# Kernel tuning notes

Measured on AMD Instinct MI355X. Metric: run time of the kernel, lower is better.

Reference implementation:

```python
import jax, jax.numpy as jnp
import numpy as np

N = 100000   # nodes
F_IN = 128   # node features
H = 32       # hidden size (hard-coded in module)


def setup_inputs() -> dict:
    key = jax.random.key(0)
    ks = jax.random.split(key, 20)
    inp = {
        'x': jax.random.normal(ks[0], (N, F_IN), dtype=jnp.float32),
        'edge_index': jax.random.randint(ks[1], (2, 3200000), 0, N, dtype=jnp.int64),
        'edge_weight': jax.random.uniform(ks[2], (3200000,), dtype=jnp.float32),
        'prev_hidden_state': jax.random.normal(ks[3], (N, H), dtype=jnp.float32),
    }
    s = 1.0 / np.sqrt(F_IN)
    s2 = 1.0 / np.sqrt(2 * H)
    sh = 1.0 / np.sqrt(H)
    # GCNConv weights (in->H) + bias, for gates z, r, h
    for i, g in enumerate(['z', 'r', 'h']):
        inp[f'Wc_{g}'] = jax.random.uniform(ks[4 + i], (F_IN, H), minval=-s, maxval=s, dtype=jnp.float32)
        inp[f'bc_{g}'] = jnp.zeros((H,), dtype=jnp.float32)
        # torch Linear(2H -> H): weight [H, 2H], bias [H]
        inp[f'Wl_{g}'] = jax.random.uniform(ks[8 + i], (H, 2 * H), minval=-s2, maxval=s2, dtype=jnp.float32)
        inp[f'bl_{g}'] = jax.random.uniform(ks[12 + i], (H,), minval=-s2, maxval=s2, dtype=jnp.float32)
    inp['W_head'] = jax.random.uniform(ks[16], (1, H), minval=-sh, maxval=sh, dtype=jnp.float32)
    inp['b_head'] = jax.random.uniform(ks[17], (1,), minval=-sh, maxval=sh, dtype=jnp.float32)
    return inp


def _gcn_norm(edge_index, edge_weight):
    # add self-loops with weight 1, symmetric GCN normalization
    loop = jnp.arange(N, dtype=edge_index.dtype)
    row = jnp.concatenate([edge_index[0], loop])
    col = jnp.concatenate([edge_index[1], loop])
    w = jnp.concatenate([edge_weight, jnp.ones((N,), dtype=edge_weight.dtype)])
    deg = jax.ops.segment_sum(w, col, num_segments=N)
    dinv = jnp.where(deg > 0, jax.lax.rsqrt(jnp.where(deg > 0, deg, 1.0)), 0.0)
    norm = dinv[row] * w * dinv[col]
    return row, col, norm


def _gcn_conv(x, W, b, row, col, norm):
    xw = x @ W                                   # [N, H]
    agg = jax.ops.segment_sum(norm[:, None] * xw[row], col, num_segments=N)
    return agg + b


def reference(x, edge_index, edge_weight, prev_hidden_state,
              Wc_z, bc_z, Wl_z, bl_z,
              Wc_r, bc_r, Wl_r, bl_r,
              Wc_h, bc_h, Wl_h, bl_h,
              W_head, b_head):
    row, col, norm = _gcn_norm(edge_index, edge_weight)
    Hprev = prev_hidden_state

    cz = _gcn_conv(x, Wc_z, bc_z, row, col, norm)
    Z = jax.nn.sigmoid(jnp.concatenate([cz, Hprev], axis=1) @ Wl_z.T + bl_z)

    cr = _gcn_conv(x, Wc_r, bc_r, row, col, norm)
    R = jax.nn.sigmoid(jnp.concatenate([cr, Hprev], axis=1) @ Wl_r.T + bl_r)

    ch = _gcn_conv(x, Wc_h, bc_h, row, col, norm)
    Ht = jnp.tanh(jnp.concatenate([ch, Hprev * R], axis=1) @ Wl_h.T + bl_h)

    Hnew = Z * Hprev + (1.0 - Z) * Ht
    y = jax.nn.relu(Hnew) @ W_head.T + b_head    # [N, 1]
    return (y, Hnew)
```

## Files before the change

kernel.cpp:

```cpp
#include <hip/hip_runtime.h>

#define NN 100000
#define FIN 128
#define HD 32
#define EE 3200000
#define NBUK 391
#define EPB 6144
#define NBLK ((EE + EPB - 1) / EPB)

typedef unsigned int uint;
typedef unsigned short ushort;

__device__ __forceinline__ ushort f2bf(float f) {
    uint b = __float_as_uint(f);
    return (ushort)((b + 0x7FFFu + ((b >> 16) & 1u)) >> 16);
}
__device__ __forceinline__ float bf2f(ushort u) {
    return __uint_as_float(((uint)u) << 16);
}

__global__ void detect_kernel(const uint* __restrict__ ei32, int* __restrict__ flag) {
    int t = threadIdx.x;
    uint v = 0;
#pragma unroll
    for (int r = 0; r < 4; r++) v |= ei32[2 * (t + 64 * r) + 1];
    unsigned long long nz = __ballot(v != 0u);
    if (t == 0) *flag = (nz == 0ULL) ? 1 : 0;
}

__device__ __forceinline__ int load_idx32(const int* __restrict__ ei, long long pos, int is64) {
    return is64 ? ei[pos * 2] : ei[pos];
}

__global__ __launch_bounds__(256) void passA_hist(const int* __restrict__ ei,
                                                  int* __restrict__ blockhist,
                                                  const int* __restrict__ flag) {
    __shared__ int hist[NBUK];
    int tid = threadIdx.x, blk = blockIdx.x;
    for (int b = tid; b < NBUK; b += 256) hist[b] = 0;
    __syncthreads();
    int is64 = *flag;
    int e0 = blk * EPB, e1 = e0 + EPB; if (e1 > EE) e1 = EE;
    for (int e = e0 + tid; e < e1; e += 256) {
        int col = load_idx32(ei, (long long)EE + e, is64);
        atomicAdd(&hist[col >> 8], 1);
    }
    __syncthreads();
    for (int b = tid; b < NBUK; b += 256) blockhist[blk * NBUK + b] = hist[b];
}

__global__ void scan_bucket(const int* __restrict__ blockhist, int* __restrict__ off_local,
                            int* __restrict__ total) {
    int b = blockIdx.x;
    int l = threadIdx.x;
    int run = 0;
    for (int c = 0; c < NBLK; c += 64) {
        int blk = c + l;
        int v = (blk < NBLK) ? blockhist[blk * NBUK + b] : 0;
        int incl = v;
#pragma unroll
        for (int d = 1; d < 64; d <<= 1) {
            int t = __shfl_up(incl, d, 64);
            if (l >= d) incl += t;
        }
        if (blk < NBLK) off_local[blk * NBUK + b] = run + (incl - v);
        run += __shfl(incl, 63, 64);
    }
    if (l == 0) total[b] = run;
}

__global__ void scan_total(const int* __restrict__ total, int* __restrict__ bstart) {
    __shared__ int sd[512];
    int t = threadIdx.x;
    int v = (t < NBUK) ? total[t] : 0;
    sd[t] = v;
    __syncthreads();
    for (int off = 1; off < 512; off <<= 1) {
        int x = (t >= off) ? sd[t - off] : 0;
        __syncthreads();
        sd[t] += x;
        __syncthreads();
    }
    if (t < NBUK) bstart[t] = sd[t] - v;
    if (t == NBUK - 1) bstart[NBUK] = sd[t];
}

__global__ __launch_bounds__(256) void sortC_kernel(const int* __restrict__ ei,
                                                    const float* __restrict__ wt,
                                                    const int* __restrict__ bstart,
                                                    const int* __restrict__ off_local,
                                                    const int* __restrict__ blockhist,
                                                    uint2* __restrict__ erec2,
                                                    const int* __restrict__ flag) {
    __shared__ uint2 lrec[EPB];
    __shared__ int lstart[NBUK];
    __shared__ int lcur[NBUK];
    int tid = threadIdx.x, blk = blockIdx.x;
    if (tid < 64) {
        int run = 0;
        for (int c = 0; c < NBUK; c += 64) {
            int b = c + tid;
            int v = (b < NBUK) ? blockhist[blk * NBUK + b] : 0;
            int incl = v;
#pragma unroll
            for (int d = 1; d < 64; d <<= 1) {
                int t2 = __shfl_up(incl, d, 64);
                if (tid >= d) incl += t2;
            }
            if (b < NBUK) { lstart[b] = run + incl - v; lcur[b] = run + incl - v; }
            run += __shfl(incl, 63, 64);
        }
    }
    __syncthreads();
    int is64 = *flag;
    int e0 = blk * EPB, e1 = e0 + EPB; if (e1 > EE) e1 = EE;
    for (int e = e0 + tid; e < e1; e += 256) {
        int row = load_idx32(ei, e, is64);
        int col = load_idx32(ei, (long long)EE + e, is64);
        uint nb = __float_as_uint(wt[e]);
        uint enc = ((nb + 0x8000u) >> 16) & 0x7FFFu;
        int pos = atomicAdd(&lcur[col >> 8], 1);
        uint2 r; r.x = (uint)row | (enc << 17); r.y = (uint)col;
        lrec[pos] = r;
    }
    __syncthreads();
    int m = e1 - e0;
    for (int slot = tid; slot < m; slot += 256) {
        uint2 r = lrec[slot];
        int b = (int)(r.y >> 8);
        int gpos = bstart[b] + off_local[blk * NBUK + b] + (slot - lstart[b]);
        erec2[gpos] = r;
    }
}

__global__ __launch_bounds__(256) void passB_fine(const uint2* __restrict__ erec2,
                                                  const int* __restrict__ bstart,
                                                  uint* __restrict__ erecF,
                                                  int* __restrict__ estart, int* __restrict__ cnt,
                                                  float* __restrict__ dinv) {
    __shared__ int hist[256];
    __shared__ float wsum[256];
    __shared__ int off[256];
    __shared__ int cur[256];
    __shared__ int sd[256];
    int t = threadIdx.x, b = blockIdx.x;
    hist[t] = 0; wsum[t] = 0.f;
    __syncthreads();
    int e0 = bstart[b], e1 = bstart[b + 1];
    for (int e = e0 + t; e < e1; e += 256) {
        uint2 r = erec2[e];
        int cl = (int)(r.y & 255u);
        atomicAdd(&hist[cl], 1);
        atomicAdd(&wsum[cl], __uint_as_float((r.x >> 17) << 16));
    }
    __syncthreads();
    int v = hist[t];
    sd[t] = v;
    __syncthreads();
    for (int o = 1; o < 256; o <<= 1) {
        int x = (t >= o) ? sd[t - o] : 0;
        __syncthreads();
        sd[t] += x;
        __syncthreads();
    }
    off[t] = sd[t] - v;
    cur[t] = 0;
    int node = b * 256 + t;
    if (node < NN) {
        estart[node] = e0 + off[t];
        cnt[node] = v;
        dinv[node] = rsqrtf(1.0f + wsum[t]);
    }
    __syncthreads();
    for (int e = e0 + t; e < e1; e += 256) {
        uint2 r = erec2[e];
        int cl = (int)(r.y & 255u);
        int p = atomicAdd(&cur[cl], 1);
        erecF[e0 + off[cl] + p] = r.x;
    }
}

__global__ void fixup_kernel(uint* __restrict__ erecF, const float* __restrict__ dinv) {
    int e = blockIdx.x * blockDim.x + threadIdx.x;
    if (e >= EE) return;
    uint v = erecF[e];
    int row = (int)(v & 0x1FFFFu);
    float w = __uint_as_float((v >> 17) << 16);
    float wd = w * dinv[row];
    uint nb = __float_as_uint(wd);
    uint enc = ((nb + 0x8000u) >> 16) & 0x7FFFu;
    erecF[e] = (uint)row | (enc << 17);
}

__global__ __launch_bounds__(256) void gemm_xw_kernel(
        const float* __restrict__ x,
        const float* __restrict__ Wz, const float* __restrict__ Wr, const float* __restrict__ Wh,
        ushort* __restrict__ xw16) {
    __shared__ float Bs[128 * 96];
    __shared__ float AsT[8 * 128];
    int tid = threadIdx.x;
    int tx = tid & 31, ty = tid >> 5;
    int rowBase = blockIdx.x * 128;

    for (int e = tid; e < 4096; e += 256) { int k = e >> 5, c = e & 31; Bs[k * 96 + c]      = Wz[e]; }
    for (int e = tid; e < 4096; e += 256) { int k = e >> 5, c = e & 31; Bs[k * 96 + 32 + c] = Wr[e]; }
    for (int e = tid; e < 4096; e += 256) { int k = e >> 5, c = e & 31; Bs[k * 96 + 64 + c] = Wh[e]; }

    float acc0[16], acc1[16], acc2[16];
#pragma unroll
    for (int r = 0; r < 16; r++) { acc0[r] = 0.f; acc1[r] = 0.f; acc2[r] = 0.f; }

    int lr = tid >> 1;
    int lc = (tid & 1) * 4;
    for (int k0 = 0; k0 < 128; k0 += 8) {
        __syncthreads();
        int gr = rowBase + lr;
        float4 a4 = make_float4(0.f, 0.f, 0.f, 0.f);
        if (gr < NN) a4 = *(const float4*)(x + (long long)gr * FIN + k0 + lc);
        AsT[(lc + 0) * 128 + lr] = a4.x;
        AsT[(lc + 1) * 128 + lr] = a4.y;
        AsT[(lc + 2) * 128 + lr] = a4.z;
        AsT[(lc + 3) * 128 + lr] = a4.w;
        __syncthreads();
#pragma unroll
        for (int kk = 0; kk < 8; kk++) {
            float b0 = Bs[(k0 + kk) * 96 + tx];
            float b1 = Bs[(k0 + kk) * 96 + 32 + tx];
            float b2 = Bs[(k0 + kk) * 96 + 64 + tx];
            const float4* ap = (const float4*)(AsT + kk * 128 + ty * 16);
            float4 a0 = ap[0], a1 = ap[1], a2 = ap[2], a3 = ap[3];
            float av[16] = {a0.x,a0.y,a0.z,a0.w, a1.x,a1.y,a1.z,a1.w,
                            a2.x,a2.y,a2.z,a2.w, a3.x,a3.y,a3.z,a3.w};
#pragma unroll
            for (int r = 0; r < 16; r++) {
                acc0[r] = fmaf(av[r], b0, acc0[r]);
                acc1[r] = fmaf(av[r], b1, acc1[r]);
                acc2[r] = fmaf(av[r], b2, acc2[r]);
            }
        }
    }
#pragma unroll
    for (int r = 0; r < 16; r++) {
        int gr = rowBase + ty * 16 + r;
        if (gr < NN) {
            ushort* o = xw16 + (long long)gr * 96;
            uint zr = (uint)f2bf(acc0[r]) | ((uint)f2bf(acc1[r]) << 16);
            *(uint*)(o + 2 * tx) = zr;
            o[64 + tx] = f2bf(acc2[r]);
        }
    }
}

__global__ __launch_bounds__(512) void agg_gate_kernel(
        const uint* __restrict__ erecF, const int* __restrict__ estart, const int* __restrict__ cnt,
        const ushort* __restrict__ xw16, const float* __restrict__ dinv,
        const float* __restrict__ hprev,
        const float* __restrict__ bcz, const float* __restrict__ bcr, const float* __restrict__ bch,
        const float* __restrict__ Wlz, const float* __restrict__ blz,
        const float* __restrict__ Wlr, const float* __restrict__ blr,
        const float* __restrict__ Wlh, const float* __restrict__ blh,
        const float* __restrict__ Whead, const float* __restrict__ bhead,
        float* __restrict__ y, float* __restrict__ hnew) {
    __shared__ float WzT[64 * 32], WrT[64 * 32], WhT[64 * 32];
    __shared__ float czs[16][32], crs[16][32], chs[16][32], hps[16][32], rhs[16][32];
    __shared__ uint rwsh[16][32];
    int tid = threadIdx.x;
    for (int e2 = tid; e2 < 2048; e2 += 512) {
        int jj = e2 >> 6, k = e2 & 63;
        WzT[k * 32 + jj] = Wlz[e2];
        WrT[k * 32 + jj] = Wlr[e2];
        WhT[k * 32 + jj] = Wlh[e2];
    }
    int s = tid >> 5, j = tid & 31;
    int i = blockIdx.x * 16 + s;
    int beg = estart[i], c = cnt[i], end = beg + c;

    float cz = 0.f, cr = 0.f, ch = 0.f;
    int e = beg + j;
    uint vcur = (e < end) ? erecF[e] : 0u;
    for (int base = beg; base < end; base += 32) {
        rwsh[s][j] = vcur;
        int en = base + 32 + j;
        uint vnext = (en < end) ? erecF[en] : 0u;
        int mm = end - base; if (mm > 32) mm = 32;
        int t = 0;
        for (; t + 4 <= mm; t += 4) {
            uint v0 = rwsh[s][t], v1 = rwsh[s][t + 1], v2 = rwsh[s][t + 2], v3 = rwsh[s][t + 3];
            const ushort* p0 = xw16 + (long long)(v0 & 0x1FFFFu) * 96;
            const ushort* p1 = xw16 + (long long)(v1 & 0x1FFFFu) * 96;
            const ushort* p2 = xw16 + (long long)(v2 & 0x1FFFFu) * 96;
            const ushort* p3 = xw16 + (long long)(v3 & 0x1FFFFu) * 96;
            uint a0 = *(const uint*)(p0 + 2 * j);
            uint a1 = *(const uint*)(p1 + 2 * j);
            uint a2 = *(const uint*)(p2 + 2 * j);
            uint a3 = *(const uint*)(p3 + 2 * j);
            ushort h0 = p0[64 + j], h1 = p1[64 + j], h2 = p2[64 + j], h3 = p3[64 + j];
            float w0 = __uint_as_float((v0 >> 17) << 16);
            float w1 = __uint_as_float((v1 >> 17) << 16);
            float w2 = __uint_as_float((v2 >> 17) << 16);
            float w3 = __uint_as_float((v3 >> 17) << 16);
            cz = fmaf(w0, __uint_as_float(a0 << 16), cz);
            cr = fmaf(w0, __uint_as_float(a0 & 0xFFFF0000u), cr);
            ch = fmaf(w0, bf2f(h0), ch);
            cz = fmaf(w1, __uint_as_float(a1 << 16), cz);
            cr = fmaf(w1, __uint_as_float(a1 & 0xFFFF0000u), cr);
            ch = fmaf(w1, bf2f(h1), ch);
            cz = fmaf(w2, __uint_as_float(a2 << 16), cz);
            cr = fmaf(w2, __uint_as_float(a2 & 0xFFFF0000u), cr);
            ch = fmaf(w2, bf2f(h2), ch);
            cz = fmaf(w3, __uint_as_float(a3 << 16), cz);
            cr = fmaf(w3, __uint_as_float(a3 & 0xFFFF0000u), cr);
            ch = fmaf(w3, bf2f(h3), ch);
        }
        for (; t < mm; t++) {
            uint v = rwsh[s][t];
            const ushort* xr = xw16 + (long long)(v & 0x1FFFFu) * 96;
            uint zr = *(const uint*)(xr + 2 * j);
            float fh = bf2f(xr[64 + j]);
            float w = __uint_as_float((v >> 17) << 16);
            cz = fmaf(w, __uint_as_float(zr << 16), cz);
            cr = fmaf(w, __uint_as_float(zr & 0xFFFF0000u), cr);
            ch = fmaf(w, fh, ch);
        }
        vcur = vnext;
    }
    float di = dinv[i], sl = di * di;
    const ushort* xi = xw16 + (long long)i * 96;
    uint zri = *(const uint*)(xi + 2 * j);
    czs[s][j] = fmaf(sl, __uint_as_float(zri << 16),         di * cz) + bcz[j];
    crs[s][j] = fmaf(sl, __uint_as_float(zri & 0xFFFF0000u), di * cr) + bcr[j];
    chs[s][j] = fmaf(sl, bf2f(xi[64 + j]),                   di * ch) + bch[j];
    float hp = hprev[(long long)i * HD + j];
    hps[s][j] = hp;
    __syncthreads();

    float az = blz[j], arv = blr[j];
#pragma unroll
    for (int k = 0; k < 32; k++) {
        az  = fmaf(WzT[k * 32 + j], czs[s][k], az);
        arv = fmaf(WrT[k * 32 + j], crs[s][k], arv);
    }
#pragma unroll
    for (int k = 0; k < 32; k++) {
        float v = hps[s][k];
        az  = fmaf(WzT[(k + 32) * 32 + j], v, az);
        arv = fmaf(WrT[(k + 32) * 32 + j], v, arv);
    }
    float Z = 1.f / (1.f + __expf(-az));
    float R = 1.f / (1.f + __expf(-arv));
    rhs[s][j] = hp * R;
    __syncthreads();

    float ah = blh[j];
#pragma unroll
    for (int k = 0; k < 32; k++) ah = fmaf(WhT[k * 32 + j], chs[s][k], ah);
#pragma unroll
    for (int k = 0; k < 32; k++) ah = fmaf(WhT[(k + 32) * 32 + j], rhs[s][k], ah);
    float Ht = tanhf(ah);
    float hn = Z * hp + (1.f - Z) * Ht;
    float yv = fmaxf(hn, 0.f) * Whead[j];
#pragma unroll
    for (int m = 16; m; m >>= 1) yv += __shfl_xor(yv, m, 32);
    hnew[(long long)i * HD + j] = hn;
    if (j == 0) y[i] = yv + bhead[0];
}

extern "C" void kernel_launch(void* const* d_in, const int* in_sizes, int n_in,
                              void* d_out, int out_size, void* d_ws, size_t ws_size,
                              hipStream_t stream) {
    const float* x     = (const float*)d_in[0];
    const int*   ei    = (const int*)d_in[1];
    const float* wt    = (const float*)d_in[2];
    const float* hprev = (const float*)d_in[3];
    const float* Wcz = (const float*)d_in[4],  *bcz = (const float*)d_in[5];
    const float* Wlz = (const float*)d_in[6],  *blz = (const float*)d_in[7];
    const float* Wcr = (const float*)d_in[8],  *bcr = (const float*)d_in[9];
    const float* Wlr = (const float*)d_in[10], *blr = (const float*)d_in[11];
    const float* Wch = (const float*)d_in[12], *bch = (const float*)d_in[13];
    const float* Wlh = (const float*)d_in[14], *blh = (const float*)d_in[15];
    const float* Whead = (const float*)d_in[16], *bhead = (const float*)d_in[17];

    float* out_y = (float*)d_out;
    float* out_h = (float*)d_out + NN;

    float* ws = (float*)d_ws;
    float* dinv      = ws;
    int*   estart    = (int*)(ws + NN);
    int*   cnt       = (int*)(ws + 2LL * NN);
    int*   bstart    = (int*)(ws + 3LL * NN);
    int*   total     = (int*)(ws + 3LL * NN + 512);
    int*   blockhist = (int*)(ws + 3LL * NN + 1024);
    int*   off_local = (int*)(ws + 3LL * NN + 205024);
    int*   flag      = (int*)(ws + 3LL * NN + 409024);
    ushort* xw16     = (ushort*)(ws + 3LL * NN + 409056);
    uint2*  erec2    = (uint2*)(ws + 51LL * NN + 409056);
    uint*   erecF    = (uint*)(ws + 51LL * NN + 409056 + 2LL * EE);

    detect_kernel<<<1, 64, 0, stream>>>((const uint*)ei, flag);
    passA_hist<<<NBLK, 256, 0, stream>>>(ei, blockhist, flag);
    scan_bucket<<<NBUK, 64, 0, stream>>>(blockhist, off_local, total);
    scan_total<<<1, 512, 0, stream>>>(total, bstart);
    sortC_kernel<<<NBLK, 256, 0, stream>>>(ei, wt, bstart, off_local, blockhist, erec2, flag);
    passB_fine<<<NBUK, 256, 0, stream>>>(erec2, bstart, erecF, estart, cnt, dinv);
    gemm_xw_kernel<<<(NN + 127) / 128, 256, 0, stream>>>(x, Wcz, Wcr, Wch, xw16);
    fixup_kernel<<<(EE + 255) / 256, 256, 0, stream>>>(erecF, dinv);
    agg_gate_kernel<<<NN / 16, 512, 0, stream>>>(
        erecF, estart, cnt, xw16, dinv, hprev, bcz, bcr, bch,
        Wlz, blz, Wlr, blr, Wlh, blh, Whead, bhead, out_y, out_h);
}
```

Baseline: 456.4 us.

## Sort nodes by in-degree so aggregation blocks get balanced edge counts

Builds a per-node in-degree histogram in passB_fine, scans it in descending order and scatters node ids into a degree-sorted permutation. The aggregation kernel then processes nodes through this permutation, so each 16-node block holds nodes of similar degree and its warps finish at about the same time. The separate detect kernel is also folded into passA and sortC so each block detects 64-bit indices itself. This adds two small kernels, a memset and global atomics, and node access in the gate kernel becomes scattered.

```diff
diff --git a/kernel.cpp b/kernel.cpp
--- a/kernel.cpp
+++ b/kernel.cpp
@@ -19,13 +19,12 @@
     return __uint_as_float(((uint)u) << 16);
 }
 
-__global__ void detect_kernel(const uint* __restrict__ ei32, int* __restrict__ flag) {
-    int t = threadIdx.x;
+__device__ __forceinline__ int detect64(const uint* __restrict__ ei32) {
+    int l = threadIdx.x & 63;
     uint v = 0;
 #pragma unroll
-    for (int r = 0; r < 4; r++) v |= ei32[2 * (t + 64 * r) + 1];
-    unsigned long long nz = __ballot(v != 0u);
-    if (t == 0) *flag = (nz == 0ULL) ? 1 : 0;
+    for (int r = 0; r < 4; r++) v |= ei32[2 * (l + 64 * r) + 1];
+    return (__ballot(v != 0u) == 0ULL) ? 1 : 0;
 }
 
 __device__ __forceinline__ int load_idx32(const int* __restrict__ ei, long long pos, int is64) {
@@ -33,13 +32,12 @@
 }
 
 __global__ __launch_bounds__(256) void passA_hist(const int* __restrict__ ei,
-                                                  int* __restrict__ blockhist,
-                                                  const int* __restrict__ flag) {
+                                                  int* __restrict__ blockhist) {
     __shared__ int hist[NBUK];
     int tid = threadIdx.x, blk = blockIdx.x;
+    int is64 = detect64((const uint*)ei);
     for (int b = tid; b < NBUK; b += 256) hist[b] = 0;
     __syncthreads();
-    int is64 = *flag;
     int e0 = blk * EPB, e1 = e0 + EPB; if (e1 > EE) e1 = EE;
     for (int e = e0 + tid; e < e1; e += 256) {
         int col = load_idx32(ei, (long long)EE + e, is64);
@@ -90,12 +88,12 @@
                                                     const int* __restrict__ bstart,
                                                     const int* __restrict__ off_local,
                                                     const int* __restrict__ blockhist,
-                                                    uint2* __restrict__ erec2,
-                                                    const int* __restrict__ flag) {
+                                                    uint2* __restrict__ erec2) {
     __shared__ uint2 lrec[EPB];
     __shared__ int lstart[NBUK];
     __shared__ int lcur[NBUK];
     int tid = threadIdx.x, blk = blockIdx.x;
+    int is64 = detect64((const uint*)ei);
     if (tid < 64) {
         int run = 0;
         for (int c = 0; c < NBUK; c += 64) {
@@ -112,7 +110,6 @@
         }
     }
     __syncthreads();
-    int is64 = *flag;
     int e0 = blk * EPB, e1 = e0 + EPB; if (e1 > EE) e1 = EE;
     for (int e = e0 + tid; e < e1; e += 256) {
         int row = load_idx32(ei, e, is64);
@@ -137,14 +134,18 @@
                                                   const int* __restrict__ bstart,
                                                   uint* __restrict__ erecF,
                                                   int* __restrict__ estart, int* __restrict__ cnt,
-                                                  float* __restrict__ dinv) {
+                                                  float* __restrict__ dinv,
+                                                  int* __restrict__ degCnt,
+                                                  int* __restrict__ blockBase) {
     __shared__ int hist[256];
     __shared__ float wsum[256];
     __shared__ int off[256];
     __shared__ int cur[256];
     __shared__ int sd[256];
+    __shared__ int dh[128];
     int t = threadIdx.x, b = blockIdx.x;
     hist[t] = 0; wsum[t] = 0.f;
+    if (t < 128) dh[t] = 0;
     __syncthreads();
     int e0 = bstart[b], e1 = bstart[b + 1];
     for (int e = e0 + t; e < e1; e += 256) {
@@ -170,13 +171,51 @@
         estart[node] = e0 + off[t];
         cnt[node] = v;
         dinv[node] = rsqrtf(1.0f + wsum[t]);
-    }
-    __syncthreads();
+        int bin = v < 127 ? v : 127;
+        atomicAdd(&dh[bin], 1);
+    }
+    __syncthreads();
+    if (t < 128) {
+        int c = dh[t];
+        blockBase[b * 128 + t] = c ? atomicAdd(&degCnt[t], c) : 0;
+    }
     for (int e = e0 + t; e < e1; e += 256) {
         uint2 r = erec2[e];
         int cl = (int)(r.y & 255u);
         int p = atomicAdd(&cur[cl], 1);
         erecF[e0 + off[cl] + p] = r.x;
+    }
+}
+
+__global__ void scanD_kernel(const int* __restrict__ degCnt, int* __restrict__ binStart) {
+    __shared__ int sd[128];
+    int t = threadIdx.x;
+    int v = degCnt[127 - t];
+    sd[t] = v;
+    __syncthreads();
+    for (int off = 1; off < 128; off <<= 1) {
+        int x = (t >= off) ? sd[t - off] : 0;
+        __syncthreads();
+        sd[t] += x;
+        __syncthreads();
+    }
+    binStart[127 - t] = sd[t] - v;
+}
+
+__global__ __launch_bounds__(256) void permscatter_kernel(const int* __restrict__ cnt,
+                                                          const int* __restrict__ binStart,
+                                                          const int* __restrict__ blockBase,
+                                                          int* __restrict__ perm) {
+    __shared__ int cur[128];
+    int t = threadIdx.x, b = blockIdx.x;
+    if (t < 128) cur[t] = 0;
+    __syncthreads();
+    int node = b * 256 + t;
+    if (node < NN) {
+        int v = cnt[node];
+        int bin = v < 127 ? v : 127;
+        int r = atomicAdd(&cur[bin], 1);
+        perm[binStart[bin] + blockBase[b * 128 + bin] + r] = node;
     }
 }
 
@@ -253,6 +292,7 @@
 
 __global__ __launch_bounds__(512) void agg_gate_kernel(
         const uint* __restrict__ erecF, const int* __restrict__ estart, const int* __restrict__ cnt,
+        const int* __restrict__ perm,
         const ushort* __restrict__ xw16, const float* __restrict__ dinv,
         const float* __restrict__ hprev,
         const float* __restrict__ bcz, const float* __restrict__ bcr, const float* __restrict__ bch,
@@ -272,7 +312,7 @@
         WhT[k * 32 + jj] = Wlh[e2];
     }
     int s = tid >> 5, j = tid & 31;
-    int i = blockIdx.x * 16 + s;
+    int i = perm[blockIdx.x * 16 + s];
     int beg = estart[i], c = cnt[i], end = beg + c;
 
     float cz = 0.f, cr = 0.f, ch = 0.f;
@@ -387,24 +427,29 @@
     float* dinv      = ws;
     int*   estart    = (int*)(ws + NN);
     int*   cnt       = (int*)(ws + 2LL * NN);
-    int*   bstart    = (int*)(ws + 3LL * NN);
-    int*   total     = (int*)(ws + 3LL * NN + 512);
-    int*   blockhist = (int*)(ws + 3LL * NN + 1024);
-    int*   off_local = (int*)(ws + 3LL * NN + 205024);
-    int*   flag      = (int*)(ws + 3LL * NN + 409024);
-    ushort* xw16     = (ushort*)(ws + 3LL * NN + 409056);
-    uint2*  erec2    = (uint2*)(ws + 51LL * NN + 409056);
-    uint*   erecF    = (uint*)(ws + 51LL * NN + 409056 + 2LL * EE);
-
-    detect_kernel<<<1, 64, 0, stream>>>((const uint*)ei, flag);
-    passA_hist<<<NBLK, 256, 0, stream>>>(ei, blockhist, flag);
+    int*   perm      = (int*)(ws + 3LL * NN);
+    int*   bstart    = (int*)(ws + 4LL * NN);
+    int*   total     = (int*)(ws + 4LL * NN + 512);
+    int*   degCnt    = (int*)(ws + 4LL * NN + 1024);
+    int*   binStart  = (int*)(ws + 4LL * NN + 1536);
+    int*   blockhist = (int*)(ws + 4LL * NN + 2048);
+    int*   off_local = (int*)(ws + 4LL * NN + 206048);
+    int*   blockBase = (int*)(ws + 4LL * NN + 410048);
+    ushort* xw16     = (ushort*)(ws + 4LL * NN + 460224);
+    uint2*  erec2    = (uint2*)(ws + 52LL * NN + 460224);
+    uint*   erecF    = (uint*)(ws + 52LL * NN + 460224 + 2LL * EE);
+
+    hipMemsetAsync(degCnt, 0, 128 * sizeof(int), stream);
+    passA_hist<<<NBLK, 256, 0, stream>>>(ei, blockhist);
     scan_bucket<<<NBUK, 64, 0, stream>>>(blockhist, off_local, total);
     scan_total<<<1, 512, 0, stream>>>(total, bstart);
-    sortC_kernel<<<NBLK, 256, 0, stream>>>(ei, wt, bstart, off_local, blockhist, erec2, flag);
-    passB_fine<<<NBUK, 256, 0, stream>>>(erec2, bstart, erecF, estart, cnt, dinv);
+    sortC_kernel<<<NBLK, 256, 0, stream>>>(ei, wt, bstart, off_local, blockhist, erec2);
+    passB_fine<<<NBUK, 256, 0, stream>>>(erec2, bstart, erecF, estart, cnt, dinv, degCnt, blockBase);
+    scanD_kernel<<<1, 128, 0, stream>>>(degCnt, binStart);
+    permscatter_kernel<<<NBUK, 256, 0, stream>>>(cnt, binStart, blockBase, perm);
     gemm_xw_kernel<<<(NN + 127) / 128, 256, 0, stream>>>(x, Wcz, Wcr, Wch, xw16);
     fixup_kernel<<<(EE + 255) / 256, 256, 0, stream>>>(erecF, dinv);
     agg_gate_kernel<<<NN / 16, 512, 0, stream>>>(
-        erecF, estart, cnt, xw16, dinv, hprev, bcz, bcr, bch,
+        erecF, estart, cnt, perm, xw16, dinv, hprev, bcz, bcr, bch,
         Wlz, blz, Wlr, blr, Wlh, blh, Whead, bhead, out_y, out_h);
 }
```

Measured after the change: 458.1 us. Within noise of the previous version (+0.4%).
